# Performance work log

Measured on AMD Instinct MI355X. Metric: run time of the kernel, lower is better.

The kernel has to match this reference:

```python
import jax, jax.numpy as jnp
import numpy as np

N = 50000   # nodes
E = 1000000 # edges
D = 64      # hidden/filter channels
G = 5       # num_gaussians (edge_attr dim, unused by math)
N_CONV = 2


def setup_inputs() -> dict:
    key = jax.random.key(0)
    ks = jax.random.split(key, 8)
    x = jax.random.normal(ks[0], (N, D), dtype=jnp.float32)
    edge_index = jax.random.randint(ks[1], (2, E), 0, N)
    edge_weight = jax.random.uniform(ks[2], (E,), dtype=jnp.float32)
    edge_attr = jax.random.normal(ks[3], (E, G), dtype=jnp.float32)
    s = 1.0 / np.sqrt(D)
    lin0_w = jax.random.normal(ks[4], (D, D), dtype=jnp.float32) * s
    lin0_b = jnp.zeros((D,), dtype=jnp.float32)
    conv_w = jax.random.normal(ks[5], (N_CONV, D, D), dtype=jnp.float32) * s
    conv_b = jnp.zeros((N_CONV, D), dtype=jnp.float32)
    return dict(x=x, edge_index=edge_index, edge_weight=edge_weight,
                edge_attr=edge_attr, lin0_w=lin0_w, lin0_b=lin0_b,
                conv_w=conv_w, conv_b=conv_b)


def reference(x, edge_index, edge_weight, edge_attr, lin0_w, lin0_b, conv_w, conv_b):
    # edge_attr is accepted by the torch forward but never used by the convs.
    src, dst = edge_index[0], edge_index[1]
    # gcn_norm (no self loops): deg = scatter_add(w, dst); norm = d^-1/2[src]*w*d^-1/2[dst]
    deg = jax.ops.segment_sum(edge_weight, dst, num_segments=N)
    deg_safe = jnp.where(deg > 0, deg, 1.0)
    dinv = jnp.where(deg > 0, jax.lax.rsqrt(deg_safe), 0.0)
    norm = dinv[src] * edge_weight * dinv[dst]  # [E]

    out = jax.nn.relu(x @ lin0_w + lin0_b)  # lin0 + relu, [N, D]
    for i in range(N_CONV):
        h = out @ conv_w[i]                              # [N, D] transform
        msg = norm[:, None] * h[src]                     # gather + scale, [E, D]
        agg = jax.ops.segment_sum(msg, dst, num_segments=N)  # scatter-add, [N, D]
        out = out + jax.nn.relu(agg + conv_b[i])         # residual + relu
    return out
```

## Files before the change

kernel.cpp:

```cpp
#include <hip/hip_runtime.h>


#define TPB 256
#define BTPB 1024
#define EPT 8
#define EPB (BTPB * EPT)
#define CAP 64
#define MAXB 1024
#define BCAP 1536

__global__ void bin_edges_lds(const int* __restrict__ src, const int* __restrict__ dst,
                              const float* __restrict__ w, int* __restrict__ bcnt,
                              int2* __restrict__ bins, int E, int NB) {
    __shared__ int hist[MAXB];
    __shared__ int gb[MAXB];
    int t = threadIdx.x;
    for (int j = t; j < NB; j += BTPB) hist[j] = 0;
    __syncthreads();
    int base = blockIdx.x * EPB;
    int2 pk[EPT];
    int bk[EPT], lr[EPT];
#pragma unroll
    for (int i = 0; i < EPT; ++i) {
        int e = base + i * BTPB + t;
        bk[i] = -1;
        if (e < E) {
            int d = dst[e];
            int b = d >> 6;
            bk[i] = b;
            pk[i] = make_int2(src[e] | ((d & 63) << 26), __float_as_int(w[e]));
            lr[i] = atomicAdd(&hist[b], 1);
        }
    }
    __syncthreads();
    for (int j = t; j < NB; j += BTPB) {
        int h = hist[j];
        gb[j] = h ? atomicAdd(&bcnt[j], h) : 0;
    }
    __syncthreads();
#pragma unroll
    for (int i = 0; i < EPT; ++i) {
        if (bk[i] >= 0) {
            int p = gb[bk[i]] + lr[i];
            if (p < BCAP) bins[(size_t)bk[i] * BCAP + p] = pk[i];
        }
    }
}

__global__ void build_rows(const int* __restrict__ bcnt, const int2* __restrict__ bins,
                           int2* __restrict__ esw, int* __restrict__ cnt,
                           float* __restrict__ dinv, int N) {
    __shared__ int cnt64[64];
    __shared__ float wsum[64];
    int b = blockIdx.x;
    int t = threadIdx.x;
    if (t < 64) { cnt64[t] = 0; wsum[t] = 0.f; }
    __syncthreads();
    int c = min(bcnt[b], BCAP);
    for (int k = t; k < c; k += TPB) {
        int2 pk = bins[(size_t)b * BCAP + k];
        int ls = (unsigned)pk.x >> 26;
        int s = pk.x & 0x03FFFFFF;
        int p = atomicAdd(&cnt64[ls], 1);
        atomicAdd(&wsum[ls], __int_as_float(pk.y));
        if (p < CAP)
            esw[((size_t)(b * 64 + ls)) * CAP + p] = make_int2(s, pk.y);
    }
    __syncthreads();
    if (t < 64) {
        int node = b * 64 + t;
        if (node < N) {
            cnt[node] = min(cnt64[t], CAP);
            float sw = wsum[t];
            dinv[node] = sw > 0.f ? rsqrtf(sw) : 0.f;
        }
    }
}

__device__ __forceinline__ ushort f32_to_bf16_rne(float f) {
    uint b = __float_as_uint(f);
    return (ushort)((b + 0x7FFFu + ((b >> 16) & 1u)) >> 16);
}

__global__ void lin0_conv_fused(const float* __restrict__ x, const float* __restrict__ W0,
                                const float* __restrict__ b0, const float* __restrict__ Wc,
                                float* __restrict__ out, ushort* __restrict__ hb, int n) {
    __shared__ float sW0[64][64];
    __shared__ float sWc[64][64];
    __shared__ float sA[32][64];
    __shared__ float sO[32][64];
    int t = threadIdx.x;
    {
        const float4* W04 = (const float4*)W0;
        const float4* Wc4 = (const float4*)Wc;
        float4* s0 = (float4*)(&sW0[0][0]);
        float4* s1 = (float4*)(&sWc[0][0]);
#pragma unroll
        for (int i = 0; i < 4; ++i) {
            s0[t + i * 256] = W04[t + i * 256];
            s1[t + i * 256] = Wc4[t + i * 256];
        }
    }
    int node0 = blockIdx.x * 32;
#pragma unroll
    for (int i = 0; i < 2; ++i) {
        int idx = t + i * 256;
        int nd = idx >> 4, ps = idx & 15;
        float4 v = make_float4(0.f, 0.f, 0.f, 0.f);
        if (node0 + nd < n) v = ((const float4*)x)[(size_t)(node0 + nd) * 16 + ps];
        ((float4*)&sA[nd][0])[ps] = v;
    }
    __syncthreads();
    int jg = t & 15;
    int np = t >> 4;
    int n0 = np * 2, n1 = n0 + 1;
    float4 acc0 = ((const float4*)b0)[jg], acc1 = acc0;
#pragma unroll 4
    for (int k = 0; k < 64; ++k) {
        float4 wv = ((float4*)&sW0[k][0])[jg];
        float a0 = sA[n0][k], a1 = sA[n1][k];
        acc0.x = fmaf(a0, wv.x, acc0.x); acc0.y = fmaf(a0, wv.y, acc0.y);
        acc0.z = fmaf(a0, wv.z, acc0.z); acc0.w = fmaf(a0, wv.w, acc0.w);
        acc1.x = fmaf(a1, wv.x, acc1.x); acc1.y = fmaf(a1, wv.y, acc1.y);
        acc1.z = fmaf(a1, wv.z, acc1.z); acc1.w = fmaf(a1, wv.w, acc1.w);
    }
    acc0.x = fmaxf(acc0.x, 0.f); acc0.y = fmaxf(acc0.y, 0.f);
    acc0.z = fmaxf(acc0.z, 0.f); acc0.w = fmaxf(acc0.w, 0.f);
    acc1.x = fmaxf(acc1.x, 0.f); acc1.y = fmaxf(acc1.y, 0.f);
    acc1.z = fmaxf(acc1.z, 0.f); acc1.w = fmaxf(acc1.w, 0.f);
    ((float4*)&sO[n0][0])[jg] = acc0;
    ((float4*)&sO[n1][0])[jg] = acc1;
    int g0 = node0 + n0, g1 = node0 + n1;
    if (g0 < n) ((float4*)out)[(size_t)g0 * 16 + jg] = acc0;
    if (g1 < n) ((float4*)out)[(size_t)g1 * 16 + jg] = acc1;
    __syncthreads();
    float4 h0 = make_float4(0.f, 0.f, 0.f, 0.f), h1 = h0;
#pragma unroll 4
    for (int k = 0; k < 64; ++k) {
        float4 wv = ((float4*)&sWc[k][0])[jg];
        float a0 = sO[n0][k], a1 = sO[n1][k];
        h0.x = fmaf(a0, wv.x, h0.x); h0.y = fmaf(a0, wv.y, h0.y);
        h0.z = fmaf(a0, wv.z, h0.z); h0.w = fmaf(a0, wv.w, h0.w);
        h1.x = fmaf(a1, wv.x, h1.x); h1.y = fmaf(a1, wv.y, h1.y);
        h1.z = fmaf(a1, wv.z, h1.z); h1.w = fmaf(a1, wv.w, h1.w);
    }
    ushort4 u0 = make_ushort4(f32_to_bf16_rne(h0.x), f32_to_bf16_rne(h0.y),
                              f32_to_bf16_rne(h0.z), f32_to_bf16_rne(h0.w));
    ushort4 u1 = make_ushort4(f32_to_bf16_rne(h1.x), f32_to_bf16_rne(h1.y),
                              f32_to_bf16_rne(h1.z), f32_to_bf16_rne(h1.w));
    if (g0 < n) ((ushort4*)hb)[(size_t)g0 * 16 + jg] = u0;
    if (g1 < n) ((ushort4*)hb)[(size_t)g1 * 16 + jg] = u1;
}

__global__ void gemm64t(const float* __restrict__ A, const float* __restrict__ W,
                        ushort* __restrict__ C, int n) {
    __shared__ float sW[64][64];
    __shared__ float sA[32][64];
    int t = threadIdx.x;
    const float4* W4 = (const float4*)W;
    float4* sW4 = (float4*)(&sW[0][0]);
#pragma unroll
    for (int i = 0; i < 4; ++i) sW4[t + i * 256] = W4[t + i * 256];
    int node0 = blockIdx.x * 32;
#pragma unroll
    for (int i = 0; i < 2; ++i) {
        int idx = t + i * 256;
        int nd = idx >> 4, ps = idx & 15;
        float4 v = make_float4(0.f, 0.f, 0.f, 0.f);
        if (node0 + nd < n) v = ((const float4*)A)[(size_t)(node0 + nd) * 16 + ps];
        ((float4*)&sA[nd][0])[ps] = v;
    }
    __syncthreads();
    int jg = t & 15;
    int np = t >> 4;
    int n0 = np * 2, n1 = n0 + 1;
    float4 acc0 = make_float4(0.f, 0.f, 0.f, 0.f), acc1 = acc0;
#pragma unroll 4
    for (int k = 0; k < 64; ++k) {
        float4 wv = ((float4*)&sW[k][0])[jg];
        float a0 = sA[n0][k], a1 = sA[n1][k];
        acc0.x = fmaf(a0, wv.x, acc0.x); acc0.y = fmaf(a0, wv.y, acc0.y);
        acc0.z = fmaf(a0, wv.z, acc0.z); acc0.w = fmaf(a0, wv.w, acc0.w);
        acc1.x = fmaf(a1, wv.x, acc1.x); acc1.y = fmaf(a1, wv.y, acc1.y);
        acc1.z = fmaf(a1, wv.z, acc1.z); acc1.w = fmaf(a1, wv.w, acc1.w);
    }
    int g0 = node0 + n0, g1 = node0 + n1;
    ushort4 u0 = make_ushort4(f32_to_bf16_rne(acc0.x), f32_to_bf16_rne(acc0.y),
                              f32_to_bf16_rne(acc0.z), f32_to_bf16_rne(acc0.w));
    ushort4 u1 = make_ushort4(f32_to_bf16_rne(acc1.x), f32_to_bf16_rne(acc1.y),
                              f32_to_bf16_rne(acc1.z), f32_to_bf16_rne(acc1.w));
    if (g0 < n) ((ushort4*)C)[(size_t)g0 * 16 + jg] = u0;
    if (g1 < n) ((ushort4*)C)[(size_t)g1 * 16 + jg] = u1;
}

template <bool FIRST>
__global__ void gather_conv4(const ushort* __restrict__ hb, const int* __restrict__ cnt,
                             int2* __restrict__ esw, const float* __restrict__ dinv,
                             const float* __restrict__ b, float* __restrict__ out, int n) {
    int wv = (blockIdx.x * TPB + threadIdx.x) >> 6;
    int lane = threadIdx.x & 63;
    int q = lane >> 4, sub = lane & 15;
    int node = wv * 4 + q;
    bool nvalid = node < n;
    int c = nvalid ? cnt[node] : 0;
    int m1 = max(c, __shfl_xor(c, 16));
    int cmax = max(m1, __shfl_xor(m1, 32));
    float dd = (FIRST && nvalid) ? dinv[node] : 0.f;
    const float2* h64 = (const float2*)hb;
    float4 acc = make_float4(0.f, 0.f, 0.f, 0.f);
    for (int base = 0; base < cmax; base += 16) {
        int idx = base + sub;
        bool v = idx < c;
        int2 pv = v ? esw[(size_t)node * CAP + idx] : make_int2(0, 0);
        float nm;
        if (FIRST) {
            nm = v ? dinv[pv.x] * __int_as_float(pv.y) * dd : 0.f;
            if (v) esw[(size_t)node * CAP + idx].y = __float_as_int(nm);
        } else {
            nm = __int_as_float(pv.y);
        }
        int m = min(cmax - base, 16);
        int j = 0;
        for (; j + 4 <= m; j += 4) {
            int s0 = __shfl(pv.x, j, 16);
            int s1 = __shfl(pv.x, j + 1, 16);
            int s2 = __shfl(pv.x, j + 2, 16);
            int s3 = __shfl(pv.x, j + 3, 16);
            float n0 = __shfl(nm, j, 16);
            float n1 = __shfl(nm, j + 1, 16);
            float n2 = __shfl(nm, j + 2, 16);
            float n3 = __shfl(nm, j + 3, 16);
            float2 f0 = h64[(size_t)s0 * 16 + sub];
            float2 f1 = h64[(size_t)s1 * 16 + sub];
            float2 f2 = h64[(size_t)s2 * 16 + sub];
            float2 f3 = h64[(size_t)s3 * 16 + sub];
            uint a, bb;
            a = __float_as_uint(f0.x); bb = __float_as_uint(f0.y);
            acc.x = fmaf(n0, __uint_as_float(a << 16), acc.x);
            acc.y = fmaf(n0, __uint_as_float(a & 0xFFFF0000u), acc.y);
            acc.z = fmaf(n0, __uint_as_float(bb << 16), acc.z);
            acc.w = fmaf(n0, __uint_as_float(bb & 0xFFFF0000u), acc.w);
            a = __float_as_uint(f1.x); bb = __float_as_uint(f1.y);
            acc.x = fmaf(n1, __uint_as_float(a << 16), acc.x);
            acc.y = fmaf(n1, __uint_as_float(a & 0xFFFF0000u), acc.y);
            acc.z = fmaf(n1, __uint_as_float(bb << 16), acc.z);
            acc.w = fmaf(n1, __uint_as_float(bb & 0xFFFF0000u), acc.w);
            a = __float_as_uint(f2.x); bb = __float_as_uint(f2.y);
            acc.x = fmaf(n2, __uint_as_float(a << 16), acc.x);
            acc.y = fmaf(n2, __uint_as_float(a & 0xFFFF0000u), acc.y);
            acc.z = fmaf(n2, __uint_as_float(bb << 16), acc.z);
            acc.w = fmaf(n2, __uint_as_float(bb & 0xFFFF0000u), acc.w);
            a = __float_as_uint(f3.x); bb = __float_as_uint(f3.y);
            acc.x = fmaf(n3, __uint_as_float(a << 16), acc.x);
            acc.y = fmaf(n3, __uint_as_float(a & 0xFFFF0000u), acc.y);
            acc.z = fmaf(n3, __uint_as_float(bb << 16), acc.z);
            acc.w = fmaf(n3, __uint_as_float(bb & 0xFFFF0000u), acc.w);
        }
        for (; j < m; ++j) {
            int s = __shfl(pv.x, j, 16);
            float nv = __shfl(nm, j, 16);
            float2 f = h64[(size_t)s * 16 + sub];
            uint a = __float_as_uint(f.x), bb = __float_as_uint(f.y);
            acc.x = fmaf(nv, __uint_as_float(a << 16), acc.x);
            acc.y = fmaf(nv, __uint_as_float(a & 0xFFFF0000u), acc.y);
            acc.z = fmaf(nv, __uint_as_float(bb << 16), acc.z);
            acc.w = fmaf(nv, __uint_as_float(bb & 0xFFFF0000u), acc.w);
        }
    }
    if (nvalid) {
        float4 bv = ((const float4*)b)[sub];
        float4* o4 = (float4*)out + (size_t)node * 16 + sub;
        float4 ov = *o4;
        ov.x = ov.x + fmaxf(acc.x + bv.x, 0.f);
        ov.y = ov.y + fmaxf(acc.y + bv.y, 0.f);
        ov.z = ov.z + fmaxf(acc.z + bv.z, 0.f);
        ov.w = ov.w + fmaxf(acc.w + bv.w, 0.f);
        *o4 = ov;
    }
}

extern "C" void kernel_launch(void* const* d_in, const int* in_sizes, int n_in,
                              void* d_out, int out_size, void* d_ws, size_t ws_size,
                              hipStream_t stream) {
    const float* x      = (const float*)d_in[0];
    const int*   ei     = (const int*)d_in[1];
    const float* ew     = (const float*)d_in[2];
    const float* lin0_w = (const float*)d_in[4];
    const float* lin0_b = (const float*)d_in[5];
    const float* conv_w = (const float*)d_in[6];
    const float* conv_b = (const float*)d_in[7];

    const int N = in_sizes[0] / 64;
    const int E = in_sizes[2];
    const int* src = ei;
    const int* dst = ei + E;
    const int NB = (N + 63) >> 6;

    char* ws = (char*)d_ws;
    size_t off = 0;
    auto alloc = [&](size_t bytes) {
        void* p = ws + off;
        off += (bytes + 255) & ~(size_t)255;
        return p;
    };
    int*    bcnt = (int*)alloc((size_t)NB * 4);
    int*    cnt  = (int*)alloc((size_t)N * 4);
    float*  dinv = (float*)alloc((size_t)N * 4);
    int2*   bins = (int2*)alloc((size_t)NB * BCAP * 8);
    int2*   esw  = (int2*)alloc((size_t)NB * 64 * CAP * 8);
    ushort* hb   = (ushort*)alloc((size_t)N * 64 * 2);

    float* out = (float*)d_out;
    int nblk_bin = (E + EPB - 1) / EPB;
    int nblk_gemm = (N + 31) / 32;
    int nblk_gather = (N + 15) / 16;

    hipMemsetAsync(bcnt, 0, (size_t)NB * 4, stream);
    bin_edges_lds<<<nblk_bin, BTPB, 0, stream>>>(src, dst, ew, bcnt, bins, E, NB);
    build_rows<<<NB, TPB, 0, stream>>>(bcnt, bins, esw, cnt, dinv, N);

    lin0_conv_fused<<<nblk_gemm, TPB, 0, stream>>>(x, lin0_w, lin0_b, conv_w, out, hb, N);
    gather_conv4<true><<<nblk_gather, TPB, 0, stream>>>(hb, cnt, esw, dinv, conv_b, out, N);

    gemm64t<<<nblk_gemm, TPB, 0, stream>>>(out, conv_w + (size_t)64 * 64, hb, N);
    gather_conv4<false><<<nblk_gather, TPB, 0, stream>>>(hb, cnt, esw, dinv,
                                                         conv_b + 64, out, N);
}
```

Baseline: 116.7 us.

## Fuse second conv transform GEMM into first gather kernel epilogue

The standalone gemm64t launch is removed. The first gather_conv4 pass now loads the next conv weight into LDS, writes its updated node rows to shared memory, and computes the bf16 transformed features for the second conv into a separate buffer. This drops one kernel launch and a full re-read of the output array, at the cost of extra LDS (16 KB of weights per block), a block-wide sync, and a 64x64 weight load per 16-node block. Edges per thread in the binning kernel also drop from 8 to 4, which doubles the number of binning blocks.

```diff
diff --git a/kernel.cpp b/kernel.cpp
--- a/kernel.cpp
+++ b/kernel.cpp
@@ -3,7 +3,7 @@
 
 #define TPB 256
 #define BTPB 1024
-#define EPT 8
+#define EPT 4
 #define EPB (BTPB * EPT)
 #define CAP 64
 #define MAXB 1024
@@ -152,61 +152,32 @@
     if (g1 < n) ((ushort4*)hb)[(size_t)g1 * 16 + jg] = u1;
 }
 
-__global__ void gemm64t(const float* __restrict__ A, const float* __restrict__ W,
-                        ushort* __restrict__ C, int n) {
-    __shared__ float sW[64][64];
-    __shared__ float sA[32][64];
+template <bool FIRST>
+__global__ void gather_conv4(const ushort* __restrict__ hb_in, const int* __restrict__ cnt,
+                             int2* __restrict__ esw, const float* __restrict__ dinv,
+                             const float* __restrict__ b, float* __restrict__ out,
+                             const float* __restrict__ Wnext, ushort* __restrict__ hb_out,
+                             int n) {
+    __shared__ float sWc[64][64];
+    __shared__ float sO[16][64];
     int t = threadIdx.x;
-    const float4* W4 = (const float4*)W;
-    float4* sW4 = (float4*)(&sW[0][0]);
-#pragma unroll
-    for (int i = 0; i < 4; ++i) sW4[t + i * 256] = W4[t + i * 256];
-    int node0 = blockIdx.x * 32;
-#pragma unroll
-    for (int i = 0; i < 2; ++i) {
-        int idx = t + i * 256;
-        int nd = idx >> 4, ps = idx & 15;
-        float4 v = make_float4(0.f, 0.f, 0.f, 0.f);
-        if (node0 + nd < n) v = ((const float4*)A)[(size_t)(node0 + nd) * 16 + ps];
-        ((float4*)&sA[nd][0])[ps] = v;
-    }
-    __syncthreads();
-    int jg = t & 15;
-    int np = t >> 4;
-    int n0 = np * 2, n1 = n0 + 1;
-    float4 acc0 = make_float4(0.f, 0.f, 0.f, 0.f), acc1 = acc0;
-#pragma unroll 4
-    for (int k = 0; k < 64; ++k) {
-        float4 wv = ((float4*)&sW[k][0])[jg];
-        float a0 = sA[n0][k], a1 = sA[n1][k];
-        acc0.x = fmaf(a0, wv.x, acc0.x); acc0.y = fmaf(a0, wv.y, acc0.y);
-        acc0.z = fmaf(a0, wv.z, acc0.z); acc0.w = fmaf(a0, wv.w, acc0.w);
-        acc1.x = fmaf(a1, wv.x, acc1.x); acc1.y = fmaf(a1, wv.y, acc1.y);
-        acc1.z = fmaf(a1, wv.z, acc1.z); acc1.w = fmaf(a1, wv.w, acc1.w);
-    }
-    int g0 = node0 + n0, g1 = node0 + n1;
-    ushort4 u0 = make_ushort4(f32_to_bf16_rne(acc0.x), f32_to_bf16_rne(acc0.y),
-                              f32_to_bf16_rne(acc0.z), f32_to_bf16_rne(acc0.w));
-    ushort4 u1 = make_ushort4(f32_to_bf16_rne(acc1.x), f32_to_bf16_rne(acc1.y),
-                              f32_to_bf16_rne(acc1.z), f32_to_bf16_rne(acc1.w));
-    if (g0 < n) ((ushort4*)C)[(size_t)g0 * 16 + jg] = u0;
-    if (g1 < n) ((ushort4*)C)[(size_t)g1 * 16 + jg] = u1;
-}
-
-template <bool FIRST>
-__global__ void gather_conv4(const ushort* __restrict__ hb, const int* __restrict__ cnt,
-                             int2* __restrict__ esw, const float* __restrict__ dinv,
-                             const float* __restrict__ b, float* __restrict__ out, int n) {
+    if (FIRST) {
+        const float4* Wc4 = (const float4*)Wnext;
+        float4* s1 = (float4*)(&sWc[0][0]);
+#pragma unroll
+        for (int i = 0; i < 4; ++i) s1[t + i * 256] = Wc4[t + i * 256];
+    }
     int wv = (blockIdx.x * TPB + threadIdx.x) >> 6;
     int lane = threadIdx.x & 63;
     int q = lane >> 4, sub = lane & 15;
     int node = wv * 4 + q;
+    int ndl = (t >> 6) * 4 + q;
     bool nvalid = node < n;
     int c = nvalid ? cnt[node] : 0;
     int m1 = max(c, __shfl_xor(c, 16));
     int cmax = max(m1, __shfl_xor(m1, 32));
     float dd = (FIRST && nvalid) ? dinv[node] : 0.f;
-    const float2* h64 = (const float2*)hb;
+    const float2* h64 = (const float2*)hb_in;
     float4 acc = make_float4(0.f, 0.f, 0.f, 0.f);
     for (int base = 0; base < cmax; base += 16) {
         int idx = base + sub;
@@ -267,15 +238,35 @@
             acc.w = fmaf(nv, __uint_as_float(bb & 0xFFFF0000u), acc.w);
         }
     }
+    float4 ov = make_float4(0.f, 0.f, 0.f, 0.f);
     if (nvalid) {
         float4 bv = ((const float4*)b)[sub];
         float4* o4 = (float4*)out + (size_t)node * 16 + sub;
-        float4 ov = *o4;
+        ov = *o4;
         ov.x = ov.x + fmaxf(acc.x + bv.x, 0.f);
         ov.y = ov.y + fmaxf(acc.y + bv.y, 0.f);
         ov.z = ov.z + fmaxf(acc.z + bv.z, 0.f);
         ov.w = ov.w + fmaxf(acc.w + bv.w, 0.f);
         *o4 = ov;
+    }
+    if (FIRST) {
+        ((float4*)&sO[ndl][0])[sub] = ov;
+        __syncthreads();
+        int nd = t >> 4, jg = t & 15;
+        float4 h = make_float4(0.f, 0.f, 0.f, 0.f);
+#pragma unroll 4
+        for (int k = 0; k < 64; ++k) {
+            float4 wv2 = ((float4*)&sWc[k][0])[jg];
+            float a0 = sO[nd][k];
+            h.x = fmaf(a0, wv2.x, h.x); h.y = fmaf(a0, wv2.y, h.y);
+            h.z = fmaf(a0, wv2.z, h.z); h.w = fmaf(a0, wv2.w, h.w);
+        }
+        int g = blockIdx.x * 16 + nd;
+        if (g < n) {
+            ushort4 u = make_ushort4(f32_to_bf16_rne(h.x), f32_to_bf16_rne(h.y),
+                                     f32_to_bf16_rne(h.z), f32_to_bf16_rne(h.w));
+            ((ushort4*)hb_out)[(size_t)g * 16 + jg] = u;
+        }
     }
 }
 
@@ -309,6 +300,7 @@
     int2*   bins = (int2*)alloc((size_t)NB * BCAP * 8);
     int2*   esw  = (int2*)alloc((size_t)NB * 64 * CAP * 8);
     ushort* hb   = (ushort*)alloc((size_t)N * 64 * 2);
+    ushort* hb2  = (ushort*)alloc((size_t)N * 64 * 2);
 
     float* out = (float*)d_out;
     int nblk_bin = (E + EPB - 1) / EPB;
@@ -320,9 +312,10 @@
     build_rows<<<NB, TPB, 0, stream>>>(bcnt, bins, esw, cnt, dinv, N);
 
     lin0_conv_fused<<<nblk_gemm, TPB, 0, stream>>>(x, lin0_w, lin0_b, conv_w, out, hb, N);
-    gather_conv4<true><<<nblk_gather, TPB, 0, stream>>>(hb, cnt, esw, dinv, conv_b, out, N);
-
-    gemm64t<<<nblk_gemm, TPB, 0, stream>>>(out, conv_w + (size_t)64 * 64, hb, N);
-    gather_conv4<false><<<nblk_gather, TPB, 0, stream>>>(hb, cnt, esw, dinv,
-                                                         conv_b + 64, out, N);
-}
+
+    gather_conv4<true><<<nblk_gather, TPB, 0, stream>>>(
+        hb, cnt, esw, dinv, conv_b, out, conv_w + (size_t)64 * 64, hb2, N);
+
+    gather_conv4<false><<<nblk_gather, TPB, 0, stream>>>(
+        hb2, cnt, esw, dinv, conv_b + 64, out, nullptr, nullptr, N);
+}
```

New measurement: 106.6 us. -8.7%, faster.
